# Optimization experiments

Measured on AMD Instinct MI355X. Metric: run time of the kernel, lower is better.

The kernel has to match this reference:

```python
import jax, jax.numpy as jnp
import numpy as np

EPSILON = 0.1
ALPHA = 0.5
N_ITER = 10
N_USERS = 100000


def setup_inputs() -> dict:
    key = jax.random.key(0)
    k1, k2, k3, k4, k5, k6 = jax.random.split(key, 6)
    B, C, F = 2048, 1024, 128
    users = jax.random.randint(k1, (B,), 0, N_USERS)
    items = jax.random.randint(k2, (B, C), 0, C)
    D = jax.random.uniform(k3, (B, C), minval=0.1, maxval=1.0)
    capacities = jax.random.uniform(k4, (C,), minval=0.5, maxval=1.5)
    # ScaledEmbedding: normal init scaled down by embedding_dim
    item_emb = jax.random.normal(k5, (C, F), dtype=jnp.float32) / F
    user_emb = jax.random.normal(k6, (N_USERS, F), dtype=jnp.float32) / F
    return dict(users=users, items=items, D=D, capacities=capacities,
                item_emb=item_emb, user_emb=user_emb)


def reference(users, items, D, capacities, item_emb, user_emb):
    B, C = D.shape
    ie = item_emb[items]            # [B, C, F] gathered candidate embeddings
    ue = user_emb[users]            # [B, F]
    dot = jnp.einsum('bcf,bf->bc', ie, ue)          # batched dot products
    affinity = (1.0 - ALPHA) * dot - ALPHA * (D / jnp.mean(D))
    K = jnp.exp(affinity / EPSILON)                 # [B, C]

    scaling = B / N_USERS
    a = jnp.ones((B,), K.dtype)
    b = capacities * scaling                        # [C]

    def step(carry, _):
        _, v = carry
        u = a / (K @ v)                             # [B]
        v_new = b / (K.T @ u)                       # [C]
        return (u, v_new), None

    (u, v), _ = jax.lax.scan(step, (a, jnp.ones((C,), K.dtype)),
                             None, length=N_ITER)
    P = K * (u[:, None] * v[None, :])               # K * outer(u, v)
    return P
```

## Files before the change

### kernel.cpp

```cpp
#include <hip/hip_runtime.h>
#include <hip/hip_fp16.h>

#define BB      2048
#define CC      1024
#define FF      128
#define NBLK    256
#define RPB     8
#define TPB     512
#define NITER   10
#define SUBR    8
#define SCALING_F (2048.0f / 100000.0f)

__device__ unsigned g_bar;
__device__ float g_meanPart[NBLK];
__device__ float g_colsum[NITER * SUBR * CC];

__device__ __forceinline__ float atomLoadF(const float* p) {
    return __hip_atomic_load(p, __ATOMIC_RELAXED, __HIP_MEMORY_SCOPE_AGENT);
}
__device__ __forceinline__ void atomStoreF(float* p, float v) {
    __hip_atomic_store(p, v, __ATOMIC_RELAXED, __HIP_MEMORY_SCOPE_AGENT);
}

__device__ __forceinline__ void grid_barrier(int tid) {
    __syncthreads();
    if (tid == 0) {
        unsigned c = __hip_atomic_fetch_add(&g_bar, 1u, __ATOMIC_RELAXED,
                                            __HIP_MEMORY_SCOPE_AGENT);
        unsigned target = (c / NBLK) * NBLK + NBLK;
        while ((int)(__hip_atomic_load(&g_bar, __ATOMIC_RELAXED,
                                       __HIP_MEMORY_SCOPE_AGENT) - target) < 0)
            ;
    }
    __syncthreads();
}

__global__ void __launch_bounds__(TPB)
fused_sinkhorn(const int* __restrict__ users, const int* __restrict__ items,
               const float* __restrict__ D, const float* __restrict__ caps,
               const float* __restrict__ iemb, const float* __restrict__ uemb,
               float* __restrict__ out) {
    const int bid = blockIdx.x, tid = threadIdx.x;
    const int r0 = bid * RPB;

    __shared__ union { float ue[RPB][FF]; float v[CC]; } uv;
    __shared__ __half dott[RPB][CC];
    __shared__ float  Kt[RPB][CC];
    __shared__ float  ush[RPB];
    __shared__ float  red[TPB / 64];
    __shared__ float  s2sh;

    const float4* Dg  = (const float4*)(D + ((size_t)r0 << 10));
    const int4*   it4 = (const int4*)(items + ((size_t)r0 << 10));
    float4 d_reg[4];
    int4   it_reg[4];
    #pragma unroll
    for (int k = 0; k < 4; ++k) d_reg[k]  = Dg[tid + k * TPB];
    #pragma unroll
    for (int k = 0; k < 4; ++k) it_reg[k] = it4[tid + k * TPB];

    const float cap0 = caps[tid]       * SCALING_F;
    const float cap1 = caps[tid + 512] * SCALING_F;

    for (int i = bid * TPB + tid; i < NITER * SUBR * CC; i += NBLK * TPB)
        atomStoreF(&g_colsum[i], 0.0f);

    if (tid < 256) {
        int r = tid >> 5, f4 = tid & 31;
        int u = users[r0 + r];
        ((float4*)uv.ue[r])[f4] = ((const float4*)(uemb + (size_t)u * FF))[f4];
    }

    float p = 0.0f;
    #pragma unroll
    for (int k = 0; k < 4; ++k) {
        float4 d = d_reg[k];
        p += d.x + d.y + d.z + d.w;
    }
    #pragma unroll
    for (int off = 32; off > 0; off >>= 1) p += __shfl_down(p, off, 64);
    if ((tid & 63) == 0) red[tid >> 6] = p;
    __syncthreads();
    if (tid == 0) {
        float s = 0.0f;
        #pragma unroll
        for (int k = 0; k < TPB / 64; ++k) s += red[k];
        atomStoreF(&g_meanPart[bid], s);
    }

    const float4* us = (const float4*)uv.ue;
    #pragma unroll
    for (int jj = 0; jj < CC / TPB; ++jj) {
        int j = jj * TPB + tid;
        float acc[RPB] = {};
        const float4* ip = (const float4*)(iemb + (size_t)j * FF);
        for (int f4 = 0; f4 < FF / 4; ++f4) {
            float4 a = ip[f4];
            #pragma unroll
            for (int r = 0; r < RPB; ++r) {
                float4 b = us[r * (FF / 4) + f4];
                acc[r] += a.x * b.x + a.y * b.y + a.z * b.z + a.w * b.w;
            }
        }
        #pragma unroll
        for (int r = 0; r < RPB; ++r) dott[r][j] = __float2half(acc[r]);
    }

    grid_barrier(tid);

    if (tid < 64) {
        float s = 0.0f;
        #pragma unroll
        for (int k = 0; k < NBLK / 64; ++k)
            s += atomLoadF(&g_meanPart[tid + 64 * k]);
        #pragma unroll
        for (int off = 32; off > 0; off >>= 1) s += __shfl_down(s, off, 64);
        if (tid == 0) s2sh = 5.0f * (float)(BB * CC) / s;
    }
    __syncthreads();
    const float s2 = s2sh;
    float4* KtL = (float4*)Kt;
    #pragma unroll
    for (int k = 0; k < 4; ++k) {
        int    i  = tid + k * TPB;
        int4   iv = it_reg[k];
        float4 d  = d_reg[k];
        int    r  = i >> 8;
        float4 kv;
        kv.x = __expf(5.0f * __half2float(dott[r][iv.x]) - s2 * d.x);
        kv.y = __expf(5.0f * __half2float(dott[r][iv.y]) - s2 * d.y);
        kv.z = __expf(5.0f * __half2float(dott[r][iv.z]) - s2 * d.z);
        kv.w = __expf(5.0f * __half2float(dott[r][iv.w]) - s2 * d.w);
        KtL[i] = kv;
    }

    for (int t = 0; t < NITER; ++t) {
        if (t == 0) {
            uv.v[tid]       = 1.0f;
            uv.v[tid + 512] = 1.0f;
        } else {
            const float* base = g_colsum + (size_t)(t - 1) * SUBR * CC;
            float t0[SUBR], t1[SUBR];
            #pragma unroll
            for (int k = 0; k < SUBR; ++k) t0[k] = atomLoadF(&base[k * CC + tid]);
            #pragma unroll
            for (int k = 0; k < SUBR; ++k) t1[k] = atomLoadF(&base[k * CC + tid + 512]);
            float s0 = 0.0f, s1 = 0.0f;
            #pragma unroll
            for (int k = 0; k < SUBR; ++k) { s0 += t0[k]; s1 += t1[k]; }
            uv.v[tid]       = cap0 / s0;
            uv.v[tid + 512] = cap1 / s1;
        }
        __syncthreads();

        {
            int r = tid >> 6, l = tid & 63;
            const float4* kr = (const float4*)Kt[r];
            const float4* v4 = (const float4*)uv.v;
            float pp = 0.0f;
            #pragma unroll
            for (int i2 = 0; i2 < 4; ++i2) {
                float4 k = kr[l + i2 * 64], v = v4[l + i2 * 64];
                pp += k.x * v.x + k.y * v.y + k.z * v.z + k.w * v.w;
            }
            #pragma unroll
            for (int off = 32; off > 0; off >>= 1) pp += __shfl_down(pp, off, 64);
            if (l == 0) ush[r] = 1.0f / pp;
        }
        __syncthreads();

        {
            float* cb = g_colsum + ((size_t)t * SUBR + (bid & (SUBR - 1))) * CC;
            float sA = 0.0f, sB = 0.0f;
            #pragma unroll
            for (int r = 0; r < RPB; ++r) {
                sA += Kt[r][tid]       * ush[r];
                sB += Kt[r][tid + 512] * ush[r];
            }
            atomicAdd(&cb[tid],       sA);
            atomicAdd(&cb[tid + 512], sB);
        }

        grid_barrier(tid);
    }

    {
        const float* base = g_colsum + (size_t)(NITER - 1) * SUBR * CC;
        float t0[SUBR], t1[SUBR];
        #pragma unroll
        for (int k = 0; k < SUBR; ++k) t0[k] = atomLoadF(&base[k * CC + tid]);
        #pragma unroll
        for (int k = 0; k < SUBR; ++k) t1[k] = atomLoadF(&base[k * CC + tid + 512]);
        float s0 = 0.0f, s1 = 0.0f;
        #pragma unroll
        for (int k = 0; k < SUBR; ++k) { s0 += t0[k]; s1 += t1[k]; }
        uv.v[tid]       = cap0 / s0;
        uv.v[tid + 512] = cap1 / s1;
    }
    __syncthreads();

    float4* o4 = (float4*)(out + ((size_t)r0 << 10));
    #pragma unroll
    for (int k = 0; k < 4; ++k) {
        int    i  = tid + k * TPB;
        int    r  = i >> 8;
        float4 kk = KtL[i];
        float  ur = ush[r];
        float4 v  = *(const float4*)&uv.v[(i * 4) & (CC - 1)];
        float4 pv;
        pv.x = kk.x * ur * v.x;  pv.y = kk.y * ur * v.y;
        pv.z = kk.z * ur * v.z;  pv.w = kk.w * ur * v.w;
        o4[i] = pv;
    }
}

extern "C" void kernel_launch(void* const* d_in, const int* in_sizes, int n_in,
                              void* d_out, int out_size, void* d_ws, size_t ws_size,
                              hipStream_t stream) {
    const int*   users = (const int*)d_in[0];
    const int*   items = (const int*)d_in[1];
    const float* D     = (const float*)d_in[2];
    const float* caps  = (const float*)d_in[3];
    const float* iemb  = (const float*)d_in[4];
    const float* uemb  = (const float*)d_in[5];
    float* out = (float*)d_out;

    hipLaunchKernelGGL(fused_sinkhorn, dim3(NBLK), dim3(TPB), 0, stream,
                       users, items, D, caps, iemb, uemb, out);
}
```

Before: 191.0 us.

## Replace flat grid barrier with two-level tree barrier and dual-column dot loop

Replaces the single global atomic counter barrier with a hierarchical barrier: 32 blocks arrive at one of 8 padded leaf counters, the last arriver increments a root counter, and the last leaf releases a per-slot flag. The kernel derives an epoch from a launch counter so the per-slot counters stay valid across repeated launches. The aim is to cut atomic contention on one address during the 11 grid-wide syncs. Separately, the embedding dot-product loop now computes two item columns per thread at once, which reuses each shared-memory user-embedding load and adds ILP at the cost of more registers.

After: 182.5 us. 1.05x faster.

```diff
diff --git a/kernel.cpp b/kernel.cpp
--- a/kernel.cpp
+++ b/kernel.cpp
@@ -11,7 +11,15 @@
 #define SUBR    8
 #define SCALING_F (2048.0f / 100000.0f)
 
-__device__ unsigned g_bar;
+#define NLEAF   8
+#define LPB     32
+#define NSLOT   (NITER + 1)
+#define CPAD    16
+
+__device__ unsigned g_epoch;
+__device__ unsigned g_leaf[NSLOT * NLEAF * CPAD];
+__device__ unsigned g_root[NSLOT * CPAD];
+__device__ unsigned g_rel [NSLOT * CPAD];
 __device__ float g_meanPart[NBLK];
 __device__ float g_colsum[NITER * SUBR * CC];
 
@@ -21,15 +29,25 @@
 __device__ __forceinline__ void atomStoreF(float* p, float v) {
     __hip_atomic_store(p, v, __ATOMIC_RELAXED, __HIP_MEMORY_SCOPE_AGENT);
 }
-
-__device__ __forceinline__ void grid_barrier(int tid) {
+__device__ __forceinline__ unsigned atomAddU(unsigned* p) {
+    return __hip_atomic_fetch_add(p, 1u, __ATOMIC_RELAXED,
+                                  __HIP_MEMORY_SCOPE_AGENT);
+}
+
+__device__ __forceinline__ void tree_barrier(int slot, unsigned e,
+                                             int bid, int tid) {
     __syncthreads();
     if (tid == 0) {
-        unsigned c = __hip_atomic_fetch_add(&g_bar, 1u, __ATOMIC_RELAXED,
-                                            __HIP_MEMORY_SCOPE_AGENT);
-        unsigned target = (c / NBLK) * NBLK + NBLK;
-        while ((int)(__hip_atomic_load(&g_bar, __ATOMIC_RELAXED,
-                                       __HIP_MEMORY_SCOPE_AGENT) - target) < 0)
+        const int leaf = bid >> 5;
+        unsigned rl = atomAddU(&g_leaf[(slot * NLEAF + leaf) * CPAD]);
+        if (rl == e * LPB + (LPB - 1)) {
+            unsigned rr = atomAddU(&g_root[slot * CPAD]);
+            if (rr == e * NLEAF + (NLEAF - 1))
+                __hip_atomic_store(&g_rel[slot * CPAD], e + 1u,
+                                   __ATOMIC_RELAXED, __HIP_MEMORY_SCOPE_AGENT);
+        }
+        while ((int)(__hip_atomic_load(&g_rel[slot * CPAD], __ATOMIC_RELAXED,
+                                       __HIP_MEMORY_SCOPE_AGENT) - (e + 1u)) < 0)
             ;
     }
     __syncthreads();
@@ -49,6 +67,9 @@
     __shared__ float  ush[RPB];
     __shared__ float  red[TPB / 64];
     __shared__ float  s2sh;
+    __shared__ unsigned s_epoch;
+
+    if (tid == 0) s_epoch = atomAddU(&g_epoch) >> 8;
 
     const float4* Dg  = (const float4*)(D + ((size_t)r0 << 10));
     const int4*   it4 = (const int4*)(items + ((size_t)r0 << 10));
@@ -81,6 +102,7 @@
     for (int off = 32; off > 0; off >>= 1) p += __shfl_down(p, off, 64);
     if ((tid & 63) == 0) red[tid >> 6] = p;
     __syncthreads();
+    const unsigned e = s_epoch;
     if (tid == 0) {
         float s = 0.0f;
         #pragma unroll
@@ -88,25 +110,28 @@
         atomStoreF(&g_meanPart[bid], s);
     }
 
-    const float4* us = (const float4*)uv.ue;
-    #pragma unroll
-    for (int jj = 0; jj < CC / TPB; ++jj) {
-        int j = jj * TPB + tid;
-        float acc[RPB] = {};
-        const float4* ip = (const float4*)(iemb + (size_t)j * FF);
+    {
+        const float4* us  = (const float4*)uv.ue;
+        const float4* ip0 = (const float4*)(iemb + (size_t)tid * FF);
+        const float4* ip1 = (const float4*)(iemb + (size_t)(tid + 512) * FF);
+        float acc0[RPB] = {}, acc1[RPB] = {};
         for (int f4 = 0; f4 < FF / 4; ++f4) {
-            float4 a = ip[f4];
+            float4 a0 = ip0[f4], a1 = ip1[f4];
             #pragma unroll
             for (int r = 0; r < RPB; ++r) {
                 float4 b = us[r * (FF / 4) + f4];
-                acc[r] += a.x * b.x + a.y * b.y + a.z * b.z + a.w * b.w;
+                acc0[r] += a0.x * b.x + a0.y * b.y + a0.z * b.z + a0.w * b.w;
+                acc1[r] += a1.x * b.x + a1.y * b.y + a1.z * b.z + a1.w * b.w;
             }
         }
         #pragma unroll
-        for (int r = 0; r < RPB; ++r) dott[r][j] = __float2half(acc[r]);
-    }
-
-    grid_barrier(tid);
+        for (int r = 0; r < RPB; ++r) {
+            dott[r][tid]       = __float2half(acc0[r]);
+            dott[r][tid + 512] = __float2half(acc1[r]);
+        }
+    }
+
+    tree_barrier(NITER, e, bid, tid);
 
     if (tid < 64) {
         float s = 0.0f;
@@ -181,7 +206,7 @@
             atomicAdd(&cb[tid + 512], sB);
         }
 
-        grid_barrier(tid);
+        tree_barrier(t, e, bid, tid);
     }
 
     {
```
